# Kernel optimization log

Measured on AMD Instinct MI355X. Metric: run time of the kernel, lower is better.

## Reference

```python
import jax, jax.numpy as jnp
import numpy as np

B, L = 8, 2048
D_MODEL = 512
D_TYPE = 32
NUM_TYPES = 20
REG = 5.0          # regulizing_param
BETAS = (0.4, 0.3, 1.0)
EPS = 1e-6


def setup_inputs() -> dict:
    key = jax.random.key(0)
    ks = jax.random.split(key, 9)
    event_type = jax.random.randint(ks[0], (B, L), 0, NUM_TYPES + 1)  # 0 = padding idx
    event_time = jax.random.uniform(ks[1], (B, L), dtype=jnp.float32)
    arrival_times = jax.random.uniform(ks[2], (B, L), dtype=jnp.float32)
    # BiasedPositionalEmbedding: Wt = Linear(1, d_model//2, bias=False) -> weight vector [d/2]
    Wt_pos = jax.random.normal(ks[3], (D_MODEL // 2,), dtype=jnp.float32) * 0.02
    # type embedding table, padding_idx=0 row zeroed
    type_emb = jax.random.normal(ks[4], (NUM_TYPES + 1, D_TYPE), dtype=jnp.float32) * 0.02
    type_emb = type_emb.at[0].set(0.0)
    # magic_kernel params: linear maps on concat([xd_bar, xd]) (2*d_type) -> lengthscale / gate
    w_l = jax.random.normal(ks[5], (2 * D_TYPE,), dtype=jnp.float32) * 0.1
    b_l = jnp.float32(0.5)
    w_g = jax.random.normal(ks[6], (2 * D_TYPE,), dtype=jnp.float32) * 0.1
    b_g = jnp.float32(0.0)
    return {"event_type": event_type, "event_time": event_time,
            "arrival_times": arrival_times, "Wt_pos": Wt_pos, "type_emb": type_emb,
            "w_l": w_l, "b_l": b_l, "w_g": w_g, "b_g": b_g}


def _biased_pos_emb(event_time, Wt_pos):
    # phi = Wt(interval.unsqueeze(-1)) : [B,L,d/2]
    phi = event_time[..., None] * Wt_pos  # outer product with weight column
    position = jnp.arange(L, dtype=jnp.float32)[:, None]                     # [L,1]
    div_term = jnp.exp(jnp.arange(0, D_MODEL, 2, dtype=jnp.float32)
                       * (-np.log(10000.0) / D_MODEL))                       # [d/2]
    arc = (position * div_term)[None]                                        # [1,L,d/2]
    return jnp.concatenate([jnp.sin(arc + phi), jnp.cos(arc + phi)], axis=-1)  # [B,L,d]


def reference(event_type, event_time, arrival_times, Wt_pos, type_emb, w_l, b_l, w_g, b_g):
    temp_enc = _biased_pos_emb(event_time, Wt_pos)          # [B,L,d_model]
    te = type_emb[event_type]                               # [B,L,d_type]
    hidden_vector = jnp.concatenate([temp_enc, te], -1)     # num_types > 1 branch

    # pairwise time differences: xt_bar[b,i,j]=t[b,j], xt[b,i,j]=t[b,i]
    t_diff = jnp.abs(event_time[:, None, :] - event_time[:, :, None])  # [B,L,L]

    # magic_kernel on concat([xd_bar, xd]) without materializing [B,L,L,2*d_type]:
    # Linear(concat) = te[b,j] @ w[:d_type] + te[b,i] @ w[d_type:] + bias
    pa = te @ w_l[:D_TYPE]   # [B,L] (j-side)
    pb = te @ w_l[D_TYPE:]   # [B,L] (i-side)
    ga = te @ w_g[:D_TYPE]
    gb = te @ w_g[D_TYPE:]
    l = jax.nn.softplus(pa[:, None, :] + pb[:, :, None] + b_l) + EPS   # lengthscale [B,L,L]
    g = jax.nn.sigmoid(REG * (ga[:, None, :] + gb[:, :, None] + b_g))  # gate [B,L,L]
    k_se = jnp.exp(-(t_diff * t_diff) / (2.0 * l * l))
    k_ex = jnp.exp(-t_diff / l)
    scores = g * (BETAS[0] * k_se + BETAS[1] * k_ex) * BETAS[2]

    # subsequent mask: (triu(ones, 0) - 1)^2 -> 1 strictly below diagonal, 0 elsewhere;
    # masked_fill where mask==0 with 0 (softmax=False default)
    keep = jnp.tril(jnp.ones((L, L), dtype=bool), -1)[None]  # [1,L,L]
    scores = jnp.where(keep, scores, 0.0)
    return (scores, hidden_vector, t_diff)
```

## Files before the change

### kernel.cpp

```cpp
#include <hip/hip_runtime.h>
#include <stdint.h>

#define BB 8
#define LL 2048
#define DT 32
#define HID 544
#define REGP 5.0f
#define BETA0 0.4f
#define BETA1 0.3f
#define EPSV 1e-6f

typedef float v4 __attribute__((ext_vector_type(4)));

__global__ __launch_bounds__(256) void prep_k(
    const int* __restrict__ etype, const float* __restrict__ etime,
    const float* __restrict__ wtpos, const float* __restrict__ temb,
    const float* __restrict__ wl, const float* __restrict__ wg,
    const float* __restrict__ blp, const float* __restrict__ bgp,
    float* __restrict__ hidden,
    float* __restrict__ paE, float* __restrict__ pbE,
    float* __restrict__ gaE, float* __restrict__ gbE)
{
    const int r0 = blockIdx.x << 3;
    const int tid = threadIdx.x;
    const float c = -0.03597789207803197f;
    const float divt = __expf((float)tid * c);
    const float wt = wtpos[tid];
    const float bl = blp[0];
    const float bg = bgp[0];

    #pragma unroll
    for (int rr = 0; rr < 8; ++rr) {
        const int row = r0 + rr;
        const int i = row & (LL - 1);
        const float t = etime[row];
        float arc = fmaf((float)i, divt, t * wt);
        size_t hbase = (size_t)row * HID;
        __builtin_nontemporal_store(sinf(arc), hidden + hbase + tid);
        __builtin_nontemporal_store(cosf(arc), hidden + hbase + 256 + tid);

        if (tid < 32) {
            int ty = etype[row];
            float te = temb[ty * DT + tid];
            __builtin_nontemporal_store(te, hidden + hbase + 512 + tid);
            float va = te * wl[tid];
            float vb = te * wl[32 + tid];
            float vc = te * wg[tid];
            float vd = te * wg[32 + tid];
            #pragma unroll
            for (int m = 16; m > 0; m >>= 1) {
                va += __shfl_xor(va, m, 64);
                vb += __shfl_xor(vb, m, 64);
                vc += __shfl_xor(vc, m, 64);
                vd += __shfl_xor(vd, m, 64);
            }
            if (tid == 0) {
                paE[row] = __expf(va);
                pbE[row] = __expf(vb + bl);
                gaE[row] = __expf(-REGP * vc);
                gbE[row] = __expf(-REGP * (vd + bg));
            }
        }
    }
}

__global__ __launch_bounds__(256) void pair_k(
    const float* __restrict__ etime,
    const float* __restrict__ paE, const float* __restrict__ pbE,
    const float* __restrict__ gaE, const float* __restrict__ gbE,
    float* __restrict__ scores, float* __restrict__ tdiff)
{
    const int b  = blockIdx.z;
    const int i0 = blockIdx.y << 4;
    const int j0 = (blockIdx.x << 10) + (threadIdx.x << 2);
    const int rowb = b * LL;

    const v4 tj = *(const v4*)(etime + rowb + j0);
    const v4 pj = *(const v4*)(paE + rowb + j0);
    const v4 gj = *(const v4*)(gaE + rowb + j0);

    #pragma unroll 4
    for (int ii = 0; ii < 16; ++ii) {
        const int i = i0 + ii;
        const float ti  = etime[rowb + i];
        const float pbi = pbE[rowb + i];
        const float gbi = gbE[rowb + i];
        const size_t base = ((size_t)(rowb + i) << 11) + j0;

        v4 dd;
        dd.x = fabsf(tj.x - ti);
        dd.y = fabsf(tj.y - ti);
        dd.z = fabsf(tj.z - ti);
        dd.w = fabsf(tj.w - ti);
        __builtin_nontemporal_store(dd, (v4*)(tdiff + base));

        v4 sc;
        if (j0 < i) {
            float pjv[4] = {pj.x, pj.y, pj.z, pj.w};
            float gjv[4] = {gj.x, gj.y, gj.z, gj.w};
            float dv[4]  = {dd.x, dd.y, dd.z, dd.w};
            float s[4];
            #pragma unroll
            for (int e = 0; e < 4; ++e) {
                float l  = __logf(fmaf(pjv[e], pbi, 1.0f)) + EPSV;
                float rl = __builtin_amdgcn_rcpf(l);
                float u  = dv[e] * rl;
                float kse = __expf(-0.5f * u * u);
                float kex = __expf(-u);
                float g   = __builtin_amdgcn_rcpf(fmaf(gjv[e], gbi, 1.0f));
                float v   = g * fmaf(BETA0, kse, BETA1 * kex);
                s[e] = ((j0 + e) < i) ? v : 0.0f;
            }
            sc.x = s[0]; sc.y = s[1]; sc.z = s[2]; sc.w = s[3];
        } else {
            sc = (v4)(0.0f);
        }
        __builtin_nontemporal_store(sc, (v4*)(scores + base));
    }
}

extern "C" void kernel_launch(void* const* d_in, const int* in_sizes, int n_in,
                              void* d_out, int out_size, void* d_ws, size_t ws_size,
                              hipStream_t stream) {
    const int*   etype = (const int*)d_in[0];
    const float* etime = (const float*)d_in[1];
    const float* wtpos = (const float*)d_in[3];
    const float* temb  = (const float*)d_in[4];
    const float* wl    = (const float*)d_in[5];
    const float* blp   = (const float*)d_in[6];
    const float* wg    = (const float*)d_in[7];
    const float* bgp   = (const float*)d_in[8];

    float* out    = (float*)d_out;
    float* scores = out;
    float* hidden = out + (size_t)BB * LL * LL;
    float* tdiff  = hidden + (size_t)BB * LL * HID;

    float* paE = (float*)d_ws;
    float* pbE = paE + BB * LL;
    float* gaE = pbE + BB * LL;
    float* gbE = gaE + BB * LL;

    prep_k<<<BB * LL / 8, 256, 0, stream>>>(etype, etime, wtpos, temb, wl, wg,
                                            blp, bgp, hidden, paE, pbE, gaE, gbE);
    pair_k<<<dim3(2, LL / 16, BB), 256, 0, stream>>>(etime, paE, pbE, gaE, gbE,
                                                     scores, tdiff);
}
```

Baseline: 327.3 us.

## Use hardware sin/cos in prep and widen pair kernel to 8 columns per thread

```diff
diff --git a/kernel.cpp b/kernel.cpp
--- a/kernel.cpp
+++ b/kernel.cpp
@@ -1,5 +1,6 @@
 #include <hip/hip_runtime.h>
 #include <stdint.h>
+#include <math.h>
 
 #define BB 8
 #define LL 2048
@@ -12,6 +13,14 @@
 
 typedef float v4 __attribute__((ext_vector_type(4)));
 
+__device__ __forceinline__ void fast_sincos(float x, float* s, float* c) {
+    const float inv2pi = 0.15915494309189535f;
+    float r = x * inv2pi;
+    float f = r - floorf(r);
+    *s = __builtin_amdgcn_sinf(f);
+    *c = __builtin_amdgcn_cosf(f);
+}
+
 __global__ __launch_bounds__(256) void prep_k(
     const int* __restrict__ etype, const float* __restrict__ etime,
     const float* __restrict__ wtpos, const float* __restrict__ temb,
@@ -23,8 +32,8 @@
 {
     const int r0 = blockIdx.x << 3;
     const int tid = threadIdx.x;
-    const float c = -0.03597789207803197f;
-    const float divt = __expf((float)tid * c);
+    const float cdiv = -0.03597789207803197f;
+    const float divt = __expf((float)tid * cdiv);
     const float wt = wtpos[tid];
     const float bl = blp[0];
     const float bg = bgp[0];
@@ -35,9 +44,11 @@
         const int i = row & (LL - 1);
         const float t = etime[row];
         float arc = fmaf((float)i, divt, t * wt);
+        float sv, cv;
+        fast_sincos(arc, &sv, &cv);
         size_t hbase = (size_t)row * HID;
-        __builtin_nontemporal_store(sinf(arc), hidden + hbase + tid);
-        __builtin_nontemporal_store(cosf(arc), hidden + hbase + 256 + tid);
+        __builtin_nontemporal_store(sv, hidden + hbase + tid);
+        __builtin_nontemporal_store(cv, hidden + hbase + 256 + tid);
 
         if (tid < 32) {
             int ty = etype[row];
@@ -70,16 +81,28 @@
     const float* __restrict__ gaE, const float* __restrict__ gbE,
     float* __restrict__ scores, float* __restrict__ tdiff)
 {
-    const int b  = blockIdx.z;
-    const int i0 = blockIdx.y << 4;
-    const int j0 = (blockIdx.x << 10) + (threadIdx.x << 2);
+    const int b  = blockIdx.y;
+    const int i0 = blockIdx.x << 4;
+    const int j0 = threadIdx.x << 3;
     const int rowb = b * LL;
 
-    const v4 tj = *(const v4*)(etime + rowb + j0);
-    const v4 pj = *(const v4*)(paE + rowb + j0);
-    const v4 gj = *(const v4*)(gaE + rowb + j0);
+    float tj[8], pj[8], gj[8];
+    {
+        const v4 t0 = *(const v4*)(etime + rowb + j0);
+        const v4 t1 = *(const v4*)(etime + rowb + j0 + 4);
+        tj[0]=t0.x; tj[1]=t0.y; tj[2]=t0.z; tj[3]=t0.w;
+        tj[4]=t1.x; tj[5]=t1.y; tj[6]=t1.z; tj[7]=t1.w;
+        const v4 p0 = *(const v4*)(paE + rowb + j0);
+        const v4 p1 = *(const v4*)(paE + rowb + j0 + 4);
+        pj[0]=p0.x; pj[1]=p0.y; pj[2]=p0.z; pj[3]=p0.w;
+        pj[4]=p1.x; pj[5]=p1.y; pj[6]=p1.z; pj[7]=p1.w;
+        const v4 g0 = *(const v4*)(gaE + rowb + j0);
+        const v4 g1 = *(const v4*)(gaE + rowb + j0 + 4);
+        gj[0]=g0.x; gj[1]=g0.y; gj[2]=g0.z; gj[3]=g0.w;
+        gj[4]=g1.x; gj[5]=g1.y; gj[6]=g1.z; gj[7]=g1.w;
+    }
 
-    #pragma unroll 4
+    #pragma unroll 2
     for (int ii = 0; ii < 16; ++ii) {
         const int i = i0 + ii;
         const float ti  = etime[rowb + i];
@@ -87,35 +110,37 @@
         const float gbi = gbE[rowb + i];
         const size_t base = ((size_t)(rowb + i) << 11) + j0;
 
-        v4 dd;
-        dd.x = fabsf(tj.x - ti);
-        dd.y = fabsf(tj.y - ti);
-        dd.z = fabsf(tj.z - ti);
-        dd.w = fabsf(tj.w - ti);
-        __builtin_nontemporal_store(dd, (v4*)(tdiff + base));
+        float d[8];
+        #pragma unroll
+        for (int e = 0; e < 8; ++e) d[e] = fabsf(tj[e] - ti);
 
-        v4 sc;
+        v4 t0 = { d[0], d[1], d[2], d[3] };
+        v4 t1 = { d[4], d[5], d[6], d[7] };
+        __builtin_nontemporal_store(t0, (v4*)(tdiff + base));
+        __builtin_nontemporal_store(t1, (v4*)(tdiff + base + 4));
+
+        v4 s0, s1;
         if (j0 < i) {
-            float pjv[4] = {pj.x, pj.y, pj.z, pj.w};
-            float gjv[4] = {gj.x, gj.y, gj.z, gj.w};
-            float dv[4]  = {dd.x, dd.y, dd.z, dd.w};
-            float s[4];
+            float s[8];
             #pragma unroll
-            for (int e = 0; e < 4; ++e) {
-                float l  = __logf(fmaf(pjv[e], pbi, 1.0f)) + EPSV;
+            for (int e = 0; e < 8; ++e) {
+                float l  = __logf(fmaf(pj[e], pbi, 1.0f)) + EPSV;
                 float rl = __builtin_amdgcn_rcpf(l);
-                float u  = dv[e] * rl;
+                float u  = d[e] * rl;
                 float kse = __expf(-0.5f * u * u);
                 float kex = __expf(-u);
-                float g   = __builtin_amdgcn_rcpf(fmaf(gjv[e], gbi, 1.0f));
+                float g   = __builtin_amdgcn_rcpf(fmaf(gj[e], gbi, 1.0f));
                 float v   = g * fmaf(BETA0, kse, BETA1 * kex);
                 s[e] = ((j0 + e) < i) ? v : 0.0f;
             }
-            sc.x = s[0]; sc.y = s[1]; sc.z = s[2]; sc.w = s[3];
+            s0.x=s[0]; s0.y=s[1]; s0.z=s[2]; s0.w=s[3];
+            s1.x=s[4]; s1.y=s[5]; s1.z=s[6]; s1.w=s[7];
         } else {
-            sc = (v4)(0.0f);
+            s0 = (v4)(0.0f);
+            s1 = (v4)(0.0f);
         }
-        __builtin_nontemporal_store(sc, (v4*)(scores + base));
+        __builtin_nontemporal_store(s0, (v4*)(scores + base));
+        __builtin_nontemporal_store(s1, (v4*)(scores + base + 4));
     }
 }
 
@@ -143,6 +168,6 @@
 
     prep_k<<<BB * LL / 8, 256, 0, stream>>>(etype, etime, wtpos, temb, wl, wg,
                                             blp, bgp, hidden, paE, pbE, gaE, gbE);
-    pair_k<<<dim3(2, LL / 16, BB), 256, 0, stream>>>(etime, paE, pbE, gaE, gbE,
-                                                     scores, tdiff);
+    pair_k<<<dim3(LL / 16, BB), 256, 0, stream>>>(etime, paE, pbE, gaE, gbE,
+                                                  scores, tdiff);
 }
```

Result: slower. 390.9 us (+19.4%).
